# Optimization experiments

Hardware: AMD Instinct MI355X
Metric: run time of the kernel (lower is better)

The kernel has to match this reference:

```python
import jax, jax.numpy as jnp
import numpy as np

BATCH = 256
INPUT_DIM = 64
LEVELS = 100
HV_DIM = 10000


def setup_inputs() -> dict:
    key = jax.random.key(0)
    kx, kb = jax.random.split(key)
    x = jax.random.uniform(kx, (BATCH, INPUT_DIM), dtype=jnp.float32)
    base = jax.random.normal(kb, (INPUT_DIM, LEVELS, HV_DIM), dtype=jnp.float32)
    # buffer is L2-normalized along hv_dim at construction time
    base = base / jnp.linalg.norm(base, axis=-1, keepdims=True)
    return {"x": x, "base_hvs": base}


def reference(x, base_hvs):
    D, L, H = base_hvs.shape
    B = x.shape[0]
    xn = jnp.clip(x * (L - 1), 0.0, float(L - 1))          # [B, D]
    lo = jnp.floor(xn).astype(jnp.int32)                    # [B, D]
    hi = jnp.clip(lo + 1, 0, L - 1)                         # [B, D]
    alpha = xn - lo.astype(x.dtype)                         # [B, D]

    def step(acc, inputs):
        bhv, l, h, a = inputs    # bhv: [L, H], l/h/a: [B]
        hv_low = bhv[l]          # [B, H] gather
        hv_high = bhv[h]         # [B, H] gather
        a = a[:, None]
        return acc + (1.0 - a) * hv_low + a * hv_high, None

    init = jnp.zeros((B, H), dtype=x.dtype)
    encoded, _ = jax.lax.scan(step, init, (base_hvs, lo.T, hi.T, alpha.T))
    return encoded / jnp.linalg.norm(encoded, axis=-1, keepdims=True)
```

## Files before the change

kernel.cpp:

```cpp
#include <hip/hip_runtime.h>

#define BATCH   256
#define DIMS    64
#define LEVELS  100
#define HVD     10000
#define WH      64
#define NHT     157
#define DSPLIT  8
#define DPER    8
#define LSTRIDE 68

__global__ __launch_bounds__(256) void encode_kernel(
    const float* __restrict__ x,
    const float* __restrict__ base,
    float* __restrict__ partial)
{
    __shared__ float s_chunk[LEVELS * LSTRIDE];
    __shared__ int   s_lohi[DPER][BATCH];
    __shared__ float s_a[DPER][BATCH];

    const int tid   = threadIdx.x;
    const int htile = blockIdx.x;
    const int split = blockIdx.y;
    const int h0    = htile * WH;
    const int d0    = split * DPER;

    for (int k = 0; k < DPER; ++k) {
        const int dl = k;
        const int b  = tid;
        float xv = x[b * DIMS + d0 + dl];
        float xn = fminf(fmaxf(xv * (float)(LEVELS - 1), 0.0f), (float)(LEVELS - 1));
        float fl = floorf(xn);
        int   lo = (int)fl;
        int   hi = lo < LEVELS - 1 ? lo + 1 : LEVELS - 1;
        s_lohi[dl][b] = (lo * LSTRIDE) | ((hi * LSTRIDE) << 16);
        s_a[dl][b]    = xn - fl;
    }

    const int g  = tid >> 4;
    const int ci = (tid & 15) * 4;
    const int wvalid = (HVD - h0) < WH ? (HVD - h0) : WH;

    float4 acc[16];
    #pragma unroll
    for (int j = 0; j < 16; ++j) acc[j] = make_float4(0.f, 0.f, 0.f, 0.f);

    for (int dc = 0; dc < DPER; ++dc) {
        __syncthreads();

        const float* src = base + ((size_t)(d0 + dc) * LEVELS) * (size_t)HVD + h0;
        for (int i = tid; i < LEVELS * (WH / 4); i += 256) {
            const int l  = i >> 4;
            const int cc = (i & 15) * 4;
            if (cc < wvalid) {
                float4 v = *(const float4*)(src + (size_t)l * HVD + cc);
                *(float4*)(&s_chunk[l * LSTRIDE + cc]) = v;
            }
        }
        __syncthreads();

        #pragma unroll
        for (int j = 0; j < 16; ++j) {
            const int   b    = g * 16 + j;
            const int   lohi = s_lohi[dc][b];
            const float a    = s_a[dc][b];
            const int   olo  = lohi & 0xffff;
            const int   ohi  = lohi >> 16;
            const float wl   = 1.0f - a;
            float4 vlo = *(const float4*)(&s_chunk[olo + ci]);
            float4 vhi = *(const float4*)(&s_chunk[ohi + ci]);
            acc[j].x += wl * vlo.x + a * vhi.x;
            acc[j].y += wl * vlo.y + a * vhi.y;
            acc[j].z += wl * vlo.z + a * vhi.z;
            acc[j].w += wl * vlo.w + a * vhi.w;
        }
    }

    if (ci < wvalid) {
        float* dst = partial + ((size_t)split * BATCH) * (size_t)HVD + h0 + ci;
        #pragma unroll
        for (int j = 0; j < 16; ++j) {
            const int b = g * 16 + j;
            *(float4*)(dst + (size_t)b * HVD) = acc[j];
        }
    }
}

__global__ __launch_bounds__(256) void finish_kernel(
    const float* __restrict__ partial,
    float* __restrict__ out)
{
    const int b   = blockIdx.x;
    const int tid = threadIdx.x;

    float ss = 0.f;
    for (int i = tid; i < HVD / 4; i += 256) {
        float4 s = make_float4(0.f, 0.f, 0.f, 0.f);
        #pragma unroll
        for (int sp = 0; sp < DSPLIT; ++sp) {
            const float4 v = *(const float4*)(partial +
                ((size_t)sp * BATCH + b) * (size_t)HVD + i * 4);
            s.x += v.x; s.y += v.y; s.z += v.z; s.w += v.w;
        }
        *(float4*)(out + (size_t)b * HVD + i * 4) = s;
        ss += s.x * s.x + s.y * s.y + s.z * s.z + s.w * s.w;
    }

    __shared__ float red[256];
    red[tid] = ss;
    __syncthreads();
    #pragma unroll
    for (int s = 128; s > 0; s >>= 1) {
        if (tid < s) red[tid] += red[tid + s];
        __syncthreads();
    }
    const float inv = rsqrtf(red[0]);

    for (int i = tid; i < HVD / 4; i += 256) {
        float4 v = *(float4*)(out + (size_t)b * HVD + i * 4);
        v.x *= inv; v.y *= inv; v.z *= inv; v.w *= inv;
        *(float4*)(out + (size_t)b * HVD + i * 4) = v;
    }
}

extern "C" void kernel_launch(void* const* d_in, const int* in_sizes, int n_in,
                              void* d_out, int out_size, void* d_ws, size_t ws_size,
                              hipStream_t stream)
{
    const float* x    = (const float*)d_in[0];
    const float* base = (const float*)d_in[1];
    float*       out  = (float*)d_out;
    float*       part = (float*)d_ws;

    dim3 grid(NHT, DSPLIT);
    encode_kernel<<<grid, 256, 0, stream>>>(x, base, part);
    finish_kernel<<<BATCH, 256, 0, stream>>>(part, out);
}
```

Baseline: 428.2 us.

## Load base tiles directly into LDS and widen the H tile to 128

Doubles the hidden-dim tile per block to 128 columns and uses 512 threads. Base chunks now go straight from global memory to LDS through global_load_lds instead of staging through registers. Each thread now holds 32 batch rows of float2 accumulators. The per-batch alpha is packed as fp16 together with the lo/hi indices into one word, which cuts LDS use but lowers the precision of the interpolation weight. The LDS padding is removed, which may add bank conflicts, and the grid shrinks to 79x8 blocks, which lowers parallelism.

```diff
diff --git a/kernel.cpp b/kernel.cpp
--- a/kernel.cpp
+++ b/kernel.cpp
@@ -1,88 +1,103 @@
 #include <hip/hip_runtime.h>
+#include <hip/hip_fp16.h>
 
 #define BATCH   256
 #define DIMS    64
 #define LEVELS  100
 #define HVD     10000
-#define WH      64
-#define NHT     157
+#define WH      128
+#define NHT     79
 #define DSPLIT  8
 #define DPER    8
-#define LSTRIDE 68
+#define TPB     512
 
-__global__ __launch_bounds__(256) void encode_kernel(
+__global__ __launch_bounds__(TPB, 4) void encode_kernel(
     const float* __restrict__ x,
     const float* __restrict__ base,
     float* __restrict__ partial)
 {
-    __shared__ float s_chunk[LEVELS * LSTRIDE];
-    __shared__ int   s_lohi[DPER][BATCH];
-    __shared__ float s_a[DPER][BATCH];
+    __shared__ float    s_chunk[LEVELS * WH];
+    __shared__ unsigned s_prm[DPER][BATCH];
 
     const int tid   = threadIdx.x;
+    const int w     = tid >> 6;
+    const int lane  = tid & 63;
     const int htile = blockIdx.x;
     const int split = blockIdx.y;
     const int h0    = htile * WH;
     const int d0    = split * DPER;
+    const int wvalid = (HVD - h0) < WH ? (HVD - h0) : WH;
 
-    for (int k = 0; k < DPER; ++k) {
-        const int dl = k;
-        const int b  = tid;
+    for (int i = tid; i < DPER * BATCH; i += TPB) {
+        const int dl = i >> 8;
+        const int b  = i & 255;
         float xv = x[b * DIMS + d0 + dl];
         float xn = fminf(fmaxf(xv * (float)(LEVELS - 1), 0.0f), (float)(LEVELS - 1));
         float fl = floorf(xn);
         int   lo = (int)fl;
         int   hi = lo < LEVELS - 1 ? lo + 1 : LEVELS - 1;
-        s_lohi[dl][b] = (lo * LSTRIDE) | ((hi * LSTRIDE) << 16);
-        s_a[dl][b]    = xn - fl;
+        unsigned abits = (unsigned)__half_as_ushort(__float2half(xn - fl));
+        s_prm[dl][b] = abits | ((unsigned)lo << 16) | ((unsigned)hi << 24);
     }
 
-    const int g  = tid >> 4;
-    const int ci = (tid & 15) * 4;
-    const int wvalid = (HVD - h0) < WH ? (HVD - h0) : WH;
+    const int cix   = lane * 2;
+    const int bbase = w * 32;
+    const int srow  = lane >> 5;
+    const int scol  = (lane & 31) * 4;
 
-    float4 acc[16];
+    float2 acc[32];
     #pragma unroll
-    for (int j = 0; j < 16; ++j) acc[j] = make_float4(0.f, 0.f, 0.f, 0.f);
+    for (int j = 0; j < 32; ++j) acc[j] = make_float2(0.f, 0.f);
 
+    #pragma unroll 1
     for (int dc = 0; dc < DPER; ++dc) {
         __syncthreads();
 
         const float* src = base + ((size_t)(d0 + dc) * LEVELS) * (size_t)HVD + h0;
-        for (int i = tid; i < LEVELS * (WH / 4); i += 256) {
-            const int l  = i >> 4;
-            const int cc = (i & 15) * 4;
-            if (cc < wvalid) {
-                float4 v = *(const float4*)(src + (size_t)l * HVD + cc);
-                *(float4*)(&s_chunk[l * LSTRIDE + cc]) = v;
+        for (int p = w; p < LEVELS / 2; p += 8) {
+            const float* g = src + (size_t)(2 * p + srow) * HVD + scol;
+            if (scol < wvalid) {
+                __builtin_amdgcn_global_load_lds(
+                    (const __attribute__((address_space(1))) unsigned*)g,
+                    (__attribute__((address_space(3))) unsigned*)&s_chunk[p * 2 * WH],
+                    16, 0, 0);
             }
         }
         __syncthreads();
 
         #pragma unroll
-        for (int j = 0; j < 16; ++j) {
-            const int   b    = g * 16 + j;
-            const int   lohi = s_lohi[dc][b];
-            const float a    = s_a[dc][b];
-            const int   olo  = lohi & 0xffff;
-            const int   ohi  = lohi >> 16;
-            const float wl   = 1.0f - a;
-            float4 vlo = *(const float4*)(&s_chunk[olo + ci]);
-            float4 vhi = *(const float4*)(&s_chunk[ohi + ci]);
-            acc[j].x += wl * vlo.x + a * vhi.x;
-            acc[j].y += wl * vlo.y + a * vhi.y;
-            acc[j].z += wl * vlo.z + a * vhi.z;
-            acc[j].w += wl * vlo.w + a * vhi.w;
+        for (int jj = 0; jj < 16; ++jj) {
+            uint2 pr = *(const uint2*)&s_prm[dc][bbase + 2 * jj];
+            {
+                const unsigned pk = pr.x;
+                const float a  = __half2float(__ushort_as_half((unsigned short)(pk & 0xffffu)));
+                const int olo  = (int)((pk >> 16) & 0xffu) * WH;
+                const int ohi  = (int)(pk >> 24) * WH;
+                float2 vlo = *(const float2*)&s_chunk[olo + cix];
+                float2 vhi = *(const float2*)&s_chunk[ohi + cix];
+                const float wl = 1.0f - a;
+                acc[2 * jj].x += wl * vlo.x + a * vhi.x;
+                acc[2 * jj].y += wl * vlo.y + a * vhi.y;
+            }
+            {
+                const unsigned pk = pr.y;
+                const float a  = __half2float(__ushort_as_half((unsigned short)(pk & 0xffffu)));
+                const int olo  = (int)((pk >> 16) & 0xffu) * WH;
+                const int ohi  = (int)(pk >> 24) * WH;
+                float2 vlo = *(const float2*)&s_chunk[olo + cix];
+                float2 vhi = *(const float2*)&s_chunk[ohi + cix];
+                const float wl = 1.0f - a;
+                acc[2 * jj + 1].x += wl * vlo.x + a * vhi.x;
+                acc[2 * jj + 1].y += wl * vlo.y + a * vhi.y;
+            }
         }
     }
 
-    if (ci < wvalid) {
-        float* dst = partial + ((size_t)split * BATCH) * (size_t)HVD + h0 + ci;
+    if (cix < wvalid) {
+        float* dst = partial + ((size_t)split * BATCH) * (size_t)HVD + h0 + cix;
         #pragma unroll
-        for (int j = 0; j < 16; ++j) {
-            const int b = g * 16 + j;
-            *(float4*)(dst + (size_t)b * HVD) = acc[j];
-        }
+        for (int j = 0; j < 32; ++j)
+            *(float2*)(dst + (size_t)(bbase + j) * HVD) = acc[j];
     }
 }
 
@@ -133,6 +148,6 @@
     float*       part = (float*)d_ws;
 
     dim3 grid(NHT, DSPLIT);
-    encode_kernel<<<grid, 256, 0, stream>>>(x, base, part);
+    encode_kernel<<<grid, TPB, 0, stream>>>(x, base, part);
     finish_kernel<<<BATCH, 256, 0, stream>>>(part, out);
 }
```

New measurement: 393.1 us. -8.2%, faster.
